# Kernel tuning notes

Measured on AMD Instinct MI355X. Metric: run time of the kernel, lower is better.

Reference implementation:

```python
import jax, jax.numpy as jnp
import numpy as np

NEG = -1e30  # log-space 'zero'


def setup_inputs() -> dict:
    N, T, IDIM, V, S = 16, 1024, 512, 4096, 128
    key = jax.random.key(0)
    k0, k1, k2, k3, k4 = jax.random.split(key, 5)
    hs = jax.random.normal(k0, (N, T, IDIM), dtype=jnp.float32)
    hlens = jax.random.randint(k1, (N,), T // 2, T + 1).astype(jnp.int32)
    ys = jax.random.randint(k2, (N, S), 1, V).astype(jnp.int32)  # labels exclude blank=0
    ylens = jax.random.randint(k3, (N,), S // 2, S + 1).astype(jnp.int32)
    W = jax.random.normal(k4, (V, IDIM), dtype=jnp.float32) * 0.02
    b = jnp.zeros((V,), dtype=jnp.float32)
    return {"hs": hs, "hlens": hlens, "ys": ys, "ylens": ylens, "W": W, "b": b}


def _ctc_loss(logp, hlens, ys, ylens):
    # logp: (N, T, V) log-softmax outputs; blank index = 0
    N, T, V = logp.shape
    S = ys.shape[1]
    L = 2 * S + 1
    # extended label sequence: blank, y1, blank, y2, ..., blank
    ext = jnp.zeros((N, L), dtype=ys.dtype).at[:, 1::2].set(ys)  # (N, L)
    s_idx = jnp.arange(L)
    ext_prev2 = jnp.pad(ext, ((0, 0), (2, 0)))[:, :L]
    allow_skip = (ext != 0) & (ext != ext_prev2) & (s_idx[None, :] >= 2)  # (N, L)
    Ln = 2 * ylens + 1  # valid extended length per sample

    lpT = jnp.swapaxes(logp, 0, 1)  # (T, N, V)

    # t = 0 init
    alpha0 = jnp.full((N, L), NEG, dtype=logp.dtype)
    alpha0 = alpha0.at[:, 0].set(lpT[0, :, 0])
    alpha0 = alpha0.at[:, 1].set(jnp.take_along_axis(lpT[0], ys[:, :1], axis=1)[:, 0])

    def step(alpha, xs):
        lp_t, t = xs  # lp_t: (N, V)
        lp_ext = jnp.take_along_axis(lp_t, ext, axis=1)  # (N, L)
        a1 = alpha
        a2 = jnp.pad(alpha, ((0, 0), (1, 0)), constant_values=NEG)[:, :L]
        a3 = jnp.pad(alpha, ((0, 0), (2, 0)), constant_values=NEG)[:, :L]
        a3 = jnp.where(allow_skip, a3, NEG)
        new = jnp.logaddexp(jnp.logaddexp(a1, a2), a3) + lp_ext
        new = jnp.where(s_idx[None, :] < Ln[:, None], new, NEG)
        alpha = jnp.where((t < hlens)[:, None], new, alpha)
        return alpha, None

    ts = jnp.arange(1, T, dtype=hlens.dtype)
    alpha, _ = jax.lax.scan(step, alpha0, (lpT[1:], ts))

    end1 = jnp.take_along_axis(alpha, (Ln - 1)[:, None], axis=1)[:, 0]
    end2 = jnp.take_along_axis(alpha, (Ln - 2)[:, None], axis=1)[:, 0]
    ll = jnp.logaddexp(end1, end2)  # (N,)
    per = jnp.where(ll > -1e29, -ll, 0.0)  # zero_infinity=True
    return jnp.sum(per) / N  # reduction='sum' then divided by len(hlens)


def reference(hs, hlens, ys, ylens, W, b):
    logits = jnp.einsum('nti,vi->ntv', hs, W) + b  # (N, T, V)
    logp = jax.nn.log_softmax(logits, axis=-1)
    return _ctc_loss(logp, hlens, ys, ylens)
```

## Files before the change

### kernel.cpp

```cpp
#include <hip/hip_runtime.h>
#include <cstdint>
#include <cstddef>

using short8_t = __attribute__((ext_vector_type(8))) short;
using f32x4    = __attribute__((ext_vector_type(4))) float;
typedef unsigned short bfu16;

constexpr int   Nn   = 16;
constexpr int   Tt   = 1024;
constexpr int   IDIM = 512;
constexpr int   Vv   = 4096;
constexpr int   Ss   = 128;
constexpr int   Ll   = 2 * Ss + 1;
constexpr int   LS   = 132;
constexpr int   PST  = LS * Tt;
constexpr float NEGV = -1e30f;
constexpr float L2E  = 1.4426950408889634f;
constexpr float LN2  = 0.6931471805599453f;

__device__ __forceinline__ float fexp2(float x) { return __builtin_amdgcn_exp2f(x); }
__device__ __forceinline__ float flog2(float x) { return __builtin_amdgcn_logf(x); }

__device__ __forceinline__ float dpp_shr1(float x) {
  return __int_as_float(__builtin_amdgcn_update_dpp(
      0, __float_as_int(x), 0x138, 0xf, 0xf, true));
}
__device__ __forceinline__ float dpp_shr2(float x) {
  return dpp_shr1(dpp_shr1(x));
}

__device__ __forceinline__ float rowsum16(float s) {
  s += __int_as_float(__builtin_amdgcn_update_dpp(0, __float_as_int(s), 0x121, 0xf, 0xf, false));
  s += __int_as_float(__builtin_amdgcn_update_dpp(0, __float_as_int(s), 0x122, 0xf, 0xf, false));
  s += __int_as_float(__builtin_amdgcn_update_dpp(0, __float_as_int(s), 0x124, 0xf, 0xf, false));
  s += __int_as_float(__builtin_amdgcn_update_dpp(0, __float_as_int(s), 0x128, 0xf, 0xf, false));
  return s;
}

__device__ __forceinline__ float rowmax16(float v) {
  v = fmaxf(v, __int_as_float(__builtin_amdgcn_update_dpp(0, __float_as_int(v), 0x121, 0xf, 0xf, false)));
  v = fmaxf(v, __int_as_float(__builtin_amdgcn_update_dpp(0, __float_as_int(v), 0x122, 0xf, 0xf, false)));
  v = fmaxf(v, __int_as_float(__builtin_amdgcn_update_dpp(0, __float_as_int(v), 0x124, 0xf, 0xf, false)));
  v = fmaxf(v, __int_as_float(__builtin_amdgcn_update_dpp(0, __float_as_int(v), 0x128, 0xf, 0xf, false)));
  return v;
}

__device__ __forceinline__ bfu16 f2bf(float f) {
  unsigned int x = __float_as_uint(f);
  x = x + 0x7fffu + ((x >> 16) & 1u);
  return (bfu16)(x >> 16);
}

__device__ __forceinline__ void async16(const void* g, void* l) {
  __builtin_amdgcn_global_load_lds(
      (__attribute__((address_space(1))) void*)(g),
      (__attribute__((address_space(3))) void*)(l), 16, 0, 0);
}

__global__ void convert_zero(const float4* __restrict__ hs4,
                             const float4* __restrict__ W4,
                             ushort4* __restrict__ hsb4,
                             ushort4* __restrict__ Wb4,
                             float* __restrict__ out) {
  if (blockIdx.x == 0 && threadIdx.x == 0) out[0] = 0.f;
  const int HS4 = (Nn * Tt * IDIM) / 4;
  const int TOT = HS4 + (Vv * IDIM) / 4;
  for (int i = blockIdx.x * 256 + threadIdx.x; i < TOT; i += gridDim.x * 256) {
    float4 f;
    if (i < HS4) f = hs4[i]; else f = W4[i - HS4];
    ushort4 o;
    o.x = f2bf(f.x); o.y = f2bf(f.y); o.z = f2bf(f.z); o.w = f2bf(f.w);
    if (i < HS4) hsb4[i] = o; else Wb4[i - HS4] = o;
  }
}

__global__ void build_labels(const int* __restrict__ ys,
                             int* __restrict__ labmap,
                             int* __restrict__ extidx,
                             int* __restrict__ skipflag) {
  const int n = blockIdx.x, tid = threadIdx.x;
  int* lm = labmap + n * Vv;
  for (int v = tid; v < Vv; v += 256) lm[v] = 0x7fffffff;
  __syncthreads();
  if (tid == 0) lm[0] = 0;
  if (tid < Ss) atomicMin(&lm[ys[n * Ss + tid]], tid + 1);
  __syncthreads();
  for (int s = tid; s < Ll; s += 256) {
    int v = (s & 1) ? ys[n * Ss + ((s - 1) >> 1)] : 0;
    extidx[n * Ll + s] = lm[v];
    int allow = 0;
    if ((s & 1) && s >= 3) allow = (v != ys[n * Ss + ((s - 3) >> 1)]) ? 1 : 0;
    skipflag[n * Ll + s] = allow;
  }
  __syncthreads();
  for (int v = tid; v < Vv; v += 256)
    if (lm[v] == 0x7fffffff) lm[v] = -1;
}

__global__ __launch_bounds__(512, 2) void gemm_lse(
    const bfu16* __restrict__ A,
    const bfu16* __restrict__ B,
    const float* __restrict__ bias,
    const int*   __restrict__ labmap,
    float* __restrict__ plabT,
    float* __restrict__ psum) {
  __shared__ alignas(128) char ldsraw[131072];
  const int tid  = threadIdx.x;
  const int lane = tid & 63, wid = tid >> 6;
  const int wr = wid >> 2, wc = wid & 3;

  const int flat = blockIdx.x;
  const int wg   = (flat & 7) * 128 + (flat >> 3);
  const int bR = wg >> 4, bC = wg & 15;
  const int rowbase = bR * 256, colbase = bC * 256;

  f32x4 acc[8][4];
#pragma unroll
  for (int m = 0; m < 8; m++)
#pragma unroll
    for (int n = 0; n < 4; n++) {
      f32x4 z = {0.f, 0.f, 0.f, 0.f};
      acc[m][n] = z;
    }

  const int  sw  = wid & 3;
  const bool isB = wid >= 4;
  const char* gsrc0 = (const char*)(isB ? (const void*)B : (const void*)A)
      + (size_t)((isB ? colbase : rowbase) + sw * 64 + (lane >> 3)) * (IDIM * 2)
      + (((lane & 7) ^ ((lane >> 3) & 7)) * 16);
  char* ldst0 = ldsraw + (isB ? 32768 : 0) + sw * 8192;

  const int fr = lane & 15;
  const int g  = lane >> 4;
  const int fx = fr & 7;

  const int nsamp = bR >> 2;
  const int* lm = labmap + nsamp * Vv;
  float* plT = plabT + (size_t)nsamp * PST;
  float bc[4];
  int   slot[4];
#pragma unroll
  for (int n = 0; n < 4; n++) {
    int c = colbase + wc * 64 + n * 16 + fr;
    bc[n]   = bias[c];
    slot[n] = lm[c];
  }

  auto stage = [&](int b, int t) {
#pragma unroll
    for (int i = 0; i < 8; ++i)
      async16(gsrc0 + (size_t)t * 128 + i * 8192, ldst0 + b * 65536 + i * 1024);
  };
  auto stage1 = [&](int b, int t, int i) {
    async16(gsrc0 + (size_t)t * 128 + (size_t)i * 8192, ldst0 + b * 65536 + i * 1024);
  };

  stage(0, 0);
  stage(1, 1);

  int buf = 0;
  for (int t = 0; t < 8; ++t) {
    if (t < 7) asm volatile("s_waitcnt vmcnt(8)" ::: "memory");
    else       asm volatile("s_waitcnt vmcnt(0)" ::: "memory");
    __builtin_amdgcn_s_barrier();

    const char* Ab = ldsraw + buf * 65536;
    const char* Bb = Ab + 32768;

    short8_t a0[4], a1[4], a2[4], a3[4], b0[4], b1[4];
#pragma unroll
    for (int m = 0; m < 4; m++)
      a0[m] = *(const short8_t*)(Ab + (wr * 128 + m * 16 + fr) * 128 + ((0 + g) ^ fx) * 16);
#pragma unroll
    for (int n = 0; n < 4; n++)
      b0[n] = *(const short8_t*)(Bb + (wc * 64 + n * 16 + fr) * 128 + ((0 + g) ^ fx) * 16);
#pragma unroll
    for (int m = 0; m < 4; m++)
      a1[m] = *(const short8_t*)(Ab + (wr * 128 + (m + 4) * 16 + fr) * 128 + ((0 + g) ^ fx) * 16);

    __builtin_amdgcn_s_setprio(1);
#pragma unroll
    for (int m = 0; m < 4; m++)
#pragma unroll
      for (int n = 0; n < 4; n++)
        acc[m][n] = __builtin_amdgcn_mfma_f32_16x16x32_bf16(a0[m], b0[n], acc[m][n], 0, 0, 0);
    __builtin_amdgcn_s_setprio(0);

#pragma unroll
    for (int m = 0; m < 4; m++)
      a2[m] = *(const short8_t*)(Ab + (wr * 128 + m * 16 + fr) * 128 + ((4 + g) ^ fx) * 16);
#pragma unroll
    for (int n = 0; n < 4; n++)
      b1[n] = *(const short8_t*)(Bb + (wc * 64 + n * 16 + fr) * 128 + ((4 + g) ^ fx) * 16);

    __builtin_amdgcn_s_setprio(1);
#pragma unroll
    for (int m = 0; m < 4; m++)
#pragma unroll
      for (int n = 0; n < 4; n++)
        acc[m + 4][n] = __builtin_amdgcn_mfma_f32_16x16x32_bf16(a1[m], b0[n], acc[m + 4][n], 0, 0, 0);
    __builtin_amdgcn_s_setprio(0);

#pragma unroll
    for (int m = 0; m < 4; m++)
      a3[m] = *(const short8_t*)(Ab + (wr * 128 + (m + 4) * 16 + fr) * 128 + ((4 + g) ^ fx) * 16);

    asm volatile("s_waitcnt lgkmcnt(0)" ::: "memory");
    __builtin_amdgcn_s_barrier();

    const bool dostage = (t + 2 < 8);
    if (dostage) {
      stage1(buf, t + 2, 0); stage1(buf, t + 2, 1);
      stage1(buf, t + 2, 2); stage1(buf, t + 2, 3);
    }

    __builtin_amdgcn_s_setprio(1);
#pragma unroll
    for (int m = 0; m < 4; m++)
#pragma unroll
      for (int n = 0; n < 4; n++)
        acc[m][n] = __builtin_amdgcn_mfma_f32_16x16x32_bf16(a2[m], b1[n], acc[m][n], 0, 0, 0);
    __builtin_amdgcn_s_setprio(0);

    if (dostage) {
      stage1(buf, t + 2, 4); stage1(buf, t + 2, 5);
      stage1(buf, t + 2, 6); stage1(buf, t + 2, 7);
    }

    __builtin_amdgcn_s_setprio(1);
#pragma unroll
    for (int m = 0; m < 4; m++)
#pragma unroll
      for (int n = 0; n < 4; n++)
        acc[m + 4][n] = __builtin_amdgcn_mfma_f32_16x16x32_bf16(a3[m], b1[n], acc[m + 4][n], 0, 0, 0);
    __builtin_amdgcn_s_setprio(0);

    buf ^= 1;
  }

  const int g4 = g * 4;
#pragma unroll
  for (int m = 0; m < 8; m++) {
#pragma unroll
    for (int r = 0; r < 4; r++) {
      int row = rowbase + wr * 128 + m * 16 + g4 + r;
      int tIn = row & 1023;
      float e0 = fexp2((acc[m][0][r] + bc[0]) * L2E);
      float e1 = fexp2((acc[m][1][r] + bc[1]) * L2E);
      float e2 = fexp2((acc[m][2][r] + bc[2]) * L2E);
      float e3 = fexp2((acc[m][3][r] + bc[3]) * L2E);
      if (slot[0] >= 0) plT[(size_t)slot[0] * Tt + tIn] = e0;
      if (slot[1] >= 0) plT[(size_t)slot[1] * Tt + tIn] = e1;
      if (slot[2] >= 0) plT[(size_t)slot[2] * Tt + tIn] = e2;
      if (slot[3] >= 0) plT[(size_t)slot[3] * Tt + tIn] = e3;
      float s = rowsum16((e0 + e1) + (e2 + e3));
      if (fr == 0) {
        int pc = bC * 4 + wc;
        psum[(size_t)pc * 16384 + row] = s;
      }
    }
  }
}

__global__ void lse_reduce(const float* __restrict__ psum,
                           float* __restrict__ lse) {
  int row = blockIdx.x * 256 + threadIdx.x;
  float s = 0.f;
#pragma unroll 8
  for (int j = 0; j < 64; j++)
    s += psum[(size_t)j * 16384 + row];
  lse[row] = flog2(s) * LN2;
}

__global__ __launch_bounds__(64) void ctc_dp(
    const float* __restrict__ plabT, const float* __restrict__ lse,
    const int* __restrict__ extidx, const int* __restrict__ skipflag,
    const int* __restrict__ hlens, const int* __restrict__ ylens,
    float* __restrict__ out) {
  __shared__ float alf[264];
  const int n    = blockIdx.x;
  const int lane = threadIdx.x;
  const int hlen = hlens[n];
  const int Ln   = 2 * ylens[n] + 1;
  const int sbase = lane * 4;

  const int   e1  = extidx[n * Ll + sbase + 1];
  const int   e3  = extidx[n * Ll + sbase + 3];
  const float sk1 = skipflag[n * Ll + sbase + 1] ? 1.f : 0.f;
  const float sk3 = skipflag[n * Ll + sbase + 3] ? 1.f : 0.f;
  const float skh = (lane > 0 && skipflag[n * Ll + sbase - 1]) ? 1.f : 0.f;
  const float skz = (lane > 0 && skipflag[n * Ll + sbase - 3]) ? 1.f : 0.f;
  const float skv = (lane > 1 && skipflag[n * Ll + sbase - 5]) ? 1.f : 0.f;
  const bool  l0  = (lane == 0);
  const float m0  = (sbase + 0 < Ln) ? 1.f : 0.f;
  const float m1  = (sbase + 1 < Ln) ? 1.f : 0.f;
  const float m2  = (sbase + 2 < Ln) ? 1.f : 0.f;
  const float m3  = (sbase + 3 < Ln) ? 1.f : 0.f;
  const float m4  = (lane == 63 && Ln == 257) ? 1.f : 0.f;

  const float* pl  = plabT + (size_t)n * PST;
  const float* rb  = pl;
  const float* r1p = pl + (size_t)e1 * Tt;
  const float* r3p = pl + (size_t)e3 * Tt;
  const float* lsp = lse + n * Tt;

  float slse = 0.f;
#pragma unroll
  for (int j = 0; j < 16; j++) {
    int t = lane + 64 * j;
    float v = lsp[t];
    slse += (t < hlen) ? v : 0.f;
  }
#pragma unroll
  for (int off = 32; off; off >>= 1) slse += __shfl_xor(slse, off);

  float a0 = 0.f, a1 = 0.f, a2 = 0.f, a3 = 0.f, a4 = 0.f;
  if (l0) { a0 = rb[0]; a1 = r1p[0]; }

  int sc = 0;

  auto step1 = [&](float pb, float p1, float p3) {
    float pm1 = dpp_shr1(a3);
    float n4 = (a4 + a3) * pb;
    float n3 = (a3 + a2 + sk3 * a1) * p3;
    float n2 = (a2 + a1) * pb;
    float n1 = (a1 + a0 + sk1 * pm1) * p1;
    float n0 = (a0 + pm1) * pb;
    a0 = n0; a1 = n1; a2 = n2; a3 = n3; a4 = n4;
  };

  auto pair2 = [&](float pbA, float p1A, float p3A,
                   float pbB, float p1B, float p3B) {
    float pa3 = dpp_shr1(a3);
    float pa2 = dpp_shr1(a2);
    float pa1 = dpp_shr1(a1);
    float prA = dpp_shr1(p3A);
    float h1 = (pa3 + pa2 + skh * pa1) * prA;
    float s4 = (a4 + a3) * pbA;
    float s3 = (a3 + a2 + sk3 * a1) * p3A;
    float s2 = (a2 + a1) * pbA;
    float s1 = (a1 + a0 + sk1 * pa3) * p1A;
    float s0 = (a0 + pa3) * pbA;
    a4 = (s4 + s3) * pbB;
    a3 = (s3 + s2 + sk3 * s1) * p3B;
    a2 = (s2 + s1) * pbB;
    a1 = (s1 + s0 + sk1 * h1) * p1B;
    a0 = (s0 + h1) * pbB;
  };

  auto rescale = [&]() {
    a0 *= m0; a1 *= m1; a2 *= m2; a3 *= m3; a4 *= m4;
    float mx = fmaxf(fmaxf(a0, a1), fmaxf(a2, a3));
    mx = fmaxf(mx, a4);
    mx = rowmax16(mx);
    mx = fmaxf(mx, __shfl_xor(mx, 16));
    mx = fmaxf(mx, __shfl_xor(mx, 32));
    int ee = (int)((__float_as_uint(mx) >> 23) & 0xff) - 127;
    ee = (mx > 0.f) ? ee : 0;
    float s = __uint_as_float((unsigned)(127 - ee) << 23);
    sc += ee;
    a0 *= s; a1 *= s; a2 *= s; a3 *= s; a4 *= s;
  };

  float pb_[2][4][4], p1_[2][4][4], p3_[2][4][4];
  float hx_[2][4][3], hz_[2][4][2], hv_[2][4];

  auto loadSB = [&](int sl, int t4) {
#pragma unroll
    for (int q = 0; q < 4; q++) {
      float4 vb = *(const float4*)(rb  + t4 + 4 * q);
      float4 v1 = *(const float4*)(r1p + t4 + 4 * q);
      float4 v3 = *(const float4*)(r3p + t4 + 4 * q);
      pb_[sl][q][0] = vb.x; pb_[sl][q][1] = vb.y; pb_[sl][q][2] = vb.z; pb_[sl][q][3] = vb.w;
      p1_[sl][q][0] = v1.x; p1_[sl][q][1] = v1.y; p1_[sl][q][2] = v1.z; p1_[sl][q][3] = v1.w;
      p3_[sl][q][0] = v3.x; p3_[sl][q][1] = v3.y; p3_[sl][q][2] = v3.z; p3_[sl][q][3] = v3.w;
    }
  };

  auto haloSB = [&](int sl) {
#pragma unroll
    for (int q = 0; q < 4; q++) {
      hx_[sl][q][0] = dpp_shr1(p3_[sl][q][0]);
      hx_[sl][q][1] = dpp_shr1(p3_[sl][q][1]);
      hx_[sl][q][2] = dpp_shr1(p3_[sl][q][2]);
      hz_[sl][q][0] = dpp_shr1(p1_[sl][q][0]);
      hz_[sl][q][1] = dpp_shr1(p1_[sl][q][1]);
      hv_[sl][q]    = dpp_shr2(p3_[sl][q][0]);
    }
  };

  auto quadsSB = [&](int sl) {
#pragma unroll
    for (int q = 0; q < 4; q++) {
      float x0 = dpp_shr1(a3);
      float y0 = dpp_shr1(a2);
      float z0 = dpp_shr1(a1);
      float w0 = dpp_shr1(a0);
      float v0 = dpp_shr2(a3);
      float u0 = dpp_shr2(a2);
      float q0 = dpp_shr2(a1);

      float v1 = (v0 + u0 + skv * q0) * hv_[sl][q];
      float w1 = (w0 + v0) * pb_[sl][q][0];
      float z1 = (z0 + w0 + skz * v0) * hz_[sl][q][0];
      float y1 = (y0 + z0) * pb_[sl][q][0];
      float x1 = (x0 + y0 + skh * z0) * hx_[sl][q][0];
      float z2 = (z1 + w1 + skz * v1) * hz_[sl][q][1];
      float y2 = (y1 + z1) * pb_[sl][q][1];
      float x2 = (x1 + y1 + skh * z1) * hx_[sl][q][1];
      float x3 = (x2 + y2 + skh * z2) * hx_[sl][q][2];

      float xk[4] = {x0, x1, x2, x3};
#pragma unroll
      for (int r = 0; r < 4; r++) {
        float pb = pb_[sl][q][r], p1v = p1_[sl][q][r], p3v = p3_[sl][q][r];
        float n4 = (a4 + a3) * pb;
        float n3 = (a3 + a2 + sk3 * a1) * p3v;
        float n2 = (a2 + a1) * pb;
        float n1 = (a1 + a0 + sk1 * xk[r]) * p1v;
        float n0 = (a0 + xk[r]) * pb;
        a0 = n0; a1 = n1; a2 = n2; a3 = n3; a4 = n4;
      }
    }
  };

  const int nsteps = hlen - 1;

  int t = 1;
  while (t < 4 && t <= nsteps) {
    step1(rb[t], r1p[t], r3p[t]);
    ++t;
  }

  const int nSB = (nsteps >= 19) ? (nsteps - 3) / 16 : 0;
  int t4 = 4;
  if (nSB > 0) loadSB(0, t4);

  int done = 0;
  while (done + 2 <= nSB) {
    if (done + 1 < nSB) loadSB(1, t4 + 16);
    haloSB(0); quadsSB(0);
    if (done + 2 < nSB) loadSB(0, t4 + 32);
    haloSB(1); quadsSB(1);
    rescale();
    done += 2; t4 += 32;
  }
  if (done < nSB) {
    haloSB(0); quadsSB(0);
    rescale();
    t4 += 16;
  }
  t = 4 + 16 * nSB;

  for (; t + 1 <= nsteps; t += 2) {
    pair2(rb[t], r1p[t], r3p[t], rb[t + 1], r1p[t + 1], r3p[t + 1]);
  }
  if (t <= nsteps) {
    step1(rb[t], r1p[t], r3p[t]);
  }
  rescale();

  alf[sbase + 0] = a0; alf[sbase + 1] = a1;
  alf[sbase + 2] = a2; alf[sbase + 3] = a3;
  if (lane == 63) alf[256] = a4;
  __syncthreads();
  if (l0) {
    float sum = alf[Ln - 1] + alf[Ln - 2];
    float per = 0.f;
    if (sum > 0.f) {
      float llv = (flog2(sum) + (float)sc) * LN2 - slse;
      if (llv > -1e29f) per = -llv;
    }
    atomicAdd(out, per * (1.0f / 16.0f));
  }
}

extern "C" void kernel_launch(void* const* d_in, const int* in_sizes, int n_in,
                              void* d_out, int out_size, void* d_ws, size_t ws_size,
                              hipStream_t stream) {
  const float* hs    = (const float*)d_in[0];
  const int*   hlens = (const int*)d_in[1];
  const int*   ys    = (const int*)d_in[2];
  const int*   ylens = (const int*)d_in[3];
  const float* W     = (const float*)d_in[4];
  const float* bias  = (const float*)d_in[5];
  float*       out   = (float*)d_out;
  char*        ws    = (char*)d_ws;

  const size_t off_hsb    = 0;
  const size_t off_Wb     = off_hsb    + (size_t)Nn*Tt*IDIM*2;
  const size_t off_plab   = off_Wb     + (size_t)Vv*IDIM*2;
  const size_t off_psum   = off_plab   + (size_t)Nn*LS*Tt*4;
  const size_t off_lse    = off_psum   + (size_t)64*16384*4;
  const size_t off_labmap = off_lse    + (size_t)16384*4;
  const size_t off_extidx = off_labmap + (size_t)Nn*Vv*4;
  const size_t off_skip   = off_extidx + (size_t)((Nn*Ll*4 + 255) & ~255);

  bfu16* hsb    = (bfu16*)(ws + off_hsb);
  bfu16* Wb     = (bfu16*)(ws + off_Wb);
  float* plabT  = (float*)(ws + off_plab);
  float* psum   = (float*)(ws + off_psum);
  float* lse    = (float*)(ws + off_lse);
  int*   labmap = (int*)(ws + off_labmap);
  int*   extidx = (int*)(ws + off_extidx);
  int*   skipf  = (int*)(ws + off_skip);

  convert_zero<<<2048, 256, 0, stream>>>(
      (const float4*)hs, (const float4*)W, (ushort4*)hsb, (ushort4*)Wb, out);
  build_labels<<<16, 256, 0, stream>>>(ys, labmap, extidx, skipf);
  gemm_lse<<<1024, 512, 0, stream>>>(hsb, Wb, bias, labmap, plabT, psum);
  lse_reduce<<<64, 256, 0, stream>>>(psum, lse);
  ctc_dp<<<16, 64, 0, stream>>>(plabT, lse, extidx, skipf, hlens, ylens, out);
}
```

Before: 172.7 us.

## Scatter label probabilities into per-position time-major packed buffer for CTC DP

Instead of storing one row per unique label and having the DP gather rows through an extidx indirection, the GEMM epilogue now writes each label's exp-logit to every sequence position it occupies, in a [T][128] time-major packed layout. The CTC DP then loads one float2 per lane per timestep, contiguous across lanes, replacing two strided float4 row streams. This trades a loop of extra scattered global stores in the GEMM epilogue (and a serial single-thread label build) for coalesced loads in the latency-bound DP. Duplicate labels beyond 16 occurrences would be dropped.

```diff
diff --git a/kernel.cpp b/kernel.cpp
--- a/kernel.cpp
+++ b/kernel.cpp
@@ -14,6 +14,7 @@
 constexpr int   Ll   = 2 * Ss + 1;
 constexpr int   LS   = 132;
 constexpr int   PST  = LS * Tt;
+constexpr int   PKS  = Tt * 128;
 constexpr float NEGV = -1e30f;
 constexpr float L2E  = 1.4426950408889634f;
 constexpr float LN2  = 0.6931471805599453f;
@@ -75,34 +76,38 @@
 }
 
 __global__ void build_labels(const int* __restrict__ ys,
-                             int* __restrict__ labmap,
-                             int* __restrict__ extidx,
+                             int* __restrict__ poscnt,
+                             int* __restrict__ poslist,
                              int* __restrict__ skipflag) {
   const int n = blockIdx.x, tid = threadIdx.x;
-  int* lm = labmap + n * Vv;
-  for (int v = tid; v < Vv; v += 256) lm[v] = 0x7fffffff;
+  int* pc = poscnt + n * Vv;
+  for (int v = tid; v < Vv; v += 256) pc[v] = 0;
   __syncthreads();
-  if (tid == 0) lm[0] = 0;
-  if (tid < Ss) atomicMin(&lm[ys[n * Ss + tid]], tid + 1);
-  __syncthreads();
+  if (tid == 0) {
+    int* pl_ = poslist + (size_t)n * Vv * 16;
+    for (int j = 0; j < Ss; j++) {
+      int v = ys[n * Ss + j];
+      int k = pc[v];
+      if (k < 16) pl_[v * 16 + k] = j;
+      pc[v] = k + 1;
+    }
+  }
   for (int s = tid; s < Ll; s += 256) {
-    int v = (s & 1) ? ys[n * Ss + ((s - 1) >> 1)] : 0;
-    extidx[n * Ll + s] = lm[v];
     int allow = 0;
-    if ((s & 1) && s >= 3) allow = (v != ys[n * Ss + ((s - 3) >> 1)]) ? 1 : 0;
+    if ((s & 1) && s >= 3)
+      allow = (ys[n * Ss + ((s - 1) >> 1)] != ys[n * Ss + ((s - 3) >> 1)]) ? 1 : 0;
     skipflag[n * Ll + s] = allow;
   }
-  __syncthreads();
-  for (int v = tid; v < Vv; v += 256)
-    if (lm[v] == 0x7fffffff) lm[v] = -1;
 }
 
 __global__ __launch_bounds__(512, 2) void gemm_lse(
     const bfu16* __restrict__ A,
     const bfu16* __restrict__ B,
     const float* __restrict__ bias,
-    const int*   __restrict__ labmap,
+    const int*   __restrict__ poscnt,
+    const int*   __restrict__ poslist,
     float* __restrict__ plabT,
+    float* __restrict__ pkP,
     float* __restrict__ psum) {
   __shared__ alignas(128) char ldsraw[131072];
   const int tid  = threadIdx.x;
@@ -135,15 +140,18 @@
   const int fx = fr & 7;
 
   const int nsamp = bR >> 2;
-  const int* lm = labmap + nsamp * Vv;
-  float* plT = plabT + (size_t)nsamp * PST;
+  const int* pcn = poscnt + nsamp * Vv;
+  const int* pln = poslist + (size_t)nsamp * Vv * 16;
+  float* plT  = plabT + (size_t)nsamp * PST;
+  float* pk_n = pkP + (size_t)nsamp * PKS;
   float bc[4];
-  int   slot[4];
+  int   col[4], cntc[4];
 #pragma unroll
   for (int n = 0; n < 4; n++) {
     int c = colbase + wc * 64 + n * 16 + fr;
+    col[n]  = c;
     bc[n]   = bias[c];
-    slot[n] = lm[c];
+    cntc[n] = pcn[c];
   }
 
   auto stage = [&](int b, int t) {
@@ -245,15 +253,18 @@
     for (int r = 0; r < 4; r++) {
       int row = rowbase + wr * 128 + m * 16 + g4 + r;
       int tIn = row & 1023;
-      float e0 = fexp2((acc[m][0][r] + bc[0]) * L2E);
-      float e1 = fexp2((acc[m][1][r] + bc[1]) * L2E);
-      float e2 = fexp2((acc[m][2][r] + bc[2]) * L2E);
-      float e3 = fexp2((acc[m][3][r] + bc[3]) * L2E);
-      if (slot[0] >= 0) plT[(size_t)slot[0] * Tt + tIn] = e0;
-      if (slot[1] >= 0) plT[(size_t)slot[1] * Tt + tIn] = e1;
-      if (slot[2] >= 0) plT[(size_t)slot[2] * Tt + tIn] = e2;
-      if (slot[3] >= 0) plT[(size_t)slot[3] * Tt + tIn] = e3;
-      float s = rowsum16((e0 + e1) + (e2 + e3));
+      float ev[4];
+#pragma unroll
+      for (int j = 0; j < 4; j++) {
+        float e = fexp2((acc[m][j][r] + bc[j]) * L2E);
+        ev[j] = e;
+        if (col[j] == 0) plT[tIn] = e;
+        for (int q2 = 0; q2 < cntc[j]; q2++) {
+          int pos = pln[col[j] * 16 + q2];
+          pk_n[(size_t)tIn * 128 + pos] = e;
+        }
+      }
+      float s = rowsum16((ev[0] + ev[1]) + (ev[2] + ev[3]));
       if (fr == 0) {
         int pc = bC * 4 + wc;
         psum[(size_t)pc * 16384 + row] = s;
@@ -273,8 +284,8 @@
 }
 
 __global__ __launch_bounds__(64) void ctc_dp(
-    const float* __restrict__ plabT, const float* __restrict__ lse,
-    const int* __restrict__ extidx, const int* __restrict__ skipflag,
+    const float* __restrict__ plabT, const float* __restrict__ pkP,
+    const float* __restrict__ lse, const int* __restrict__ skipflag,
     const int* __restrict__ hlens, const int* __restrict__ ylens,
     float* __restrict__ out) {
   __shared__ float alf[264];
@@ -284,8 +295,6 @@
   const int Ln   = 2 * ylens[n] + 1;
   const int sbase = lane * 4;
 
-  const int   e1  = extidx[n * Ll + sbase + 1];
-  const int   e3  = extidx[n * Ll + sbase + 3];
   const float sk1 = skipflag[n * Ll + sbase + 1] ? 1.f : 0.f;
   const float sk3 = skipflag[n * Ll + sbase + 3] ? 1.f : 0.f;
   const float skh = (lane > 0 && skipflag[n * Ll + sbase - 1]) ? 1.f : 0.f;
@@ -298,11 +307,9 @@
   const float m3  = (sbase + 3 < Ln) ? 1.f : 0.f;
   const float m4  = (lane == 63 && Ln == 257) ? 1.f : 0.f;
 
-  const float* pl  = plabT + (size_t)n * PST;
-  const float* rb  = pl;
-  const float* r1p = pl + (size_t)e1 * Tt;
-  const float* r3p = pl + (size_t)e3 * Tt;
-  const float* lsp = lse + n * Tt;
+  const float*  rb  = plabT + (size_t)n * PST;
+  const float2* pk2 = (const float2*)(pkP + (size_t)n * PKS);
+  const float*  lsp = lse + n * Tt;
 
   float slse = 0.f;
 #pragma unroll
@@ -314,8 +321,9 @@
 #pragma unroll
   for (int off = 32; off; off >>= 1) slse += __shfl_xor(slse, off);
 
+  float2 w0 = pk2[lane];
   float a0 = 0.f, a1 = 0.f, a2 = 0.f, a3 = 0.f, a4 = 0.f;
-  if (l0) { a0 = rb[0]; a1 = r1p[0]; }
+  if (l0) { a0 = rb[0]; a1 = w0.x; }
 
   int sc = 0;
 
@@ -362,30 +370,32 @@
     a0 *= s; a1 *= s; a2 *= s; a3 *= s; a4 *= s;
   };
 
-  float pb_[2][4][4], p1_[2][4][4], p3_[2][4][4];
+  float pb_[2][4][4];
+  float p1f[2][16], p3f[2][16];
   float hx_[2][4][3], hz_[2][4][2], hv_[2][4];
 
   auto loadSB = [&](int sl, int t4) {
 #pragma unroll
     for (int q = 0; q < 4; q++) {
-      float4 vb = *(const float4*)(rb  + t4 + 4 * q);
-      float4 v1 = *(const float4*)(r1p + t4 + 4 * q);
-      float4 v3 = *(const float4*)(r3p + t4 + 4 * q);
+      float4 vb = *(const float4*)(rb + t4 + 4 * q);
       pb_[sl][q][0] = vb.x; pb_[sl][q][1] = vb.y; pb_[sl][q][2] = vb.z; pb_[sl][q][3] = vb.w;
-      p1_[sl][q][0] = v1.x; p1_[sl][q][1] = v1.y; p1_[sl][q][2] = v1.z; p1_[sl][q][3] = v1.w;
-      p3_[sl][q][0] = v3.x; p3_[sl][q][1] = v3.y; p3_[sl][q][2] = v3.z; p3_[sl][q][3] = v3.w;
+    }
+#pragma unroll
+    for (int i = 0; i < 16; i++) {
+      float2 w = pk2[(size_t)(t4 + i) * 64 + lane];
+      p1f[sl][i] = w.x; p3f[sl][i] = w.y;
     }
   };
 
   auto haloSB = [&](int sl) {
 #pragma unroll
     for (int q = 0; q < 4; q++) {
-      hx_[sl][q][0] = dpp_shr1(p3_[sl][q][0]);
-      hx_[sl][q][1] = dpp_shr1(p3_[sl][q][1]);
-      hx_[sl][q][2] = dpp_shr1(p3_[sl][q][2]);
-      hz_[sl][q][0] = dpp_shr1(p1_[sl][q][0]);
-      hz_[sl][q][1] = dpp_shr1(p1_[sl][q][1]);
-      hv_[sl][q]    = dpp_shr2(p3_[sl][q][0]);
+      hx_[sl][q][0] = dpp_shr1(p3f[sl][4 * q + 0]);
+      hx_[sl][q][1] = dpp_shr1(p3f[sl][4 * q + 1]);
+      hx_[sl][q][2] = dpp_shr1(p3f[sl][4 * q + 2]);
+      hz_[sl][q][0] = dpp_shr1(p1f[sl][4 * q + 0]);
+      hz_[sl][q][1] = dpp_shr1(p1f[sl][4 * q + 1]);
+      hv_[sl][q]    = dpp_shr2(p3f[sl][4 * q + 0]);
     }
   };
 
@@ -395,14 +405,14 @@
       float x0 = dpp_shr1(a3);
       float y0 = dpp_shr1(a2);
       float z0 = dpp_shr1(a1);
-      float w0 = dpp_shr1(a0);
+      float w0_ = dpp_shr1(a0);
       float v0 = dpp_shr2(a3);
       float u0 = dpp_shr2(a2);
       float q0 = dpp_shr2(a1);
 
       float v1 = (v0 + u0 + skv * q0) * hv_[sl][q];
-      float w1 = (w0 + v0) * pb_[sl][q][0];
-      float z1 = (z0 + w0 + skz * v0) * hz_[sl][q][0];
+      float w1 = (w0_ + v0) * pb_[sl][q][0];
+      float z1 = (z0 + w0_ + skz * v0) * hz_[sl][q][0];
       float y1 = (y0 + z0) * pb_[sl][q][0];
       float x1 = (x0 + y0 + skh * z0) * hx_[sl][q][0];
       float z2 = (z1 + w1 + skz * v1) * hz_[sl][q][1];
@@ -413,7 +423,7 @@
       float xk[4] = {x0, x1, x2, x3};
 #pragma unroll
       for (int r = 0; r < 4; r++) {
-        float pb = pb_[sl][q][r], p1v = p1_[sl][q][r], p3v = p3_[sl][q][r];
+        float pb = pb_[sl][q][r], p1v = p1f[sl][4 * q + r], p3v = p3f[sl][4 * q + r];
         float n4 = (a4 + a3) * pb;
         float n3 = (a3 + a2 + sk3 * a1) * p3v;
         float n2 = (a2 + a1) * pb;
@@ -428,7 +438,8 @@
 
   int t = 1;
   while (t < 4 && t <= nsteps) {
-    step1(rb[t], r1p[t], r3p[t]);
+    float2 w = pk2[(size_t)t * 64 + lane];
+    step1(rb[t], w.x, w.y);
     ++t;
   }
 
@@ -453,10 +464,13 @@
   t = 4 + 16 * nSB;
 
   for (; t + 1 <= nsteps; t += 2) {
-    pair2(rb[t], r1p[t], r3p[t], rb[t + 1], r1p[t + 1], r3p[t + 1]);
+    float2 wA = pk2[(size_t)t * 64 + lane];
+    float2 wB = pk2[(size_t)(t + 1) * 64 + lane];
+    pair2(rb[t], wA.x, wA.y, rb[t + 1], wB.x, wB.y);
   }
   if (t <= nsteps) {
-    step1(rb[t], r1p[t], r3p[t]);
+    float2 w = pk2[(size_t)t * 64 + lane];
+    step1(rb[t], w.x, w.y);
   }
   rescale();
 
@@ -490,25 +504,27 @@
   const size_t off_hsb    = 0;
   const size_t off_Wb     = off_hsb    + (size_t)Nn*Tt*IDIM*2;
   const size_t off_plab   = off_Wb     + (size_t)Vv*IDIM*2;
-  const size_t off_psum   = off_plab   + (size_t)Nn*LS*Tt*4;
+  const size_t off_pkP    = off_plab   + (size_t)Nn*LS*Tt*4;
+  const size_t off_psum   = off_pkP    + (size_t)Nn*Tt*128*4;
   const size_t off_lse    = off_psum   + (size_t)64*16384*4;
-  const size_t off_labmap = off_lse    + (size_t)16384*4;
-  const size_t off_extidx = off_labmap + (size_t)Nn*Vv*4;
-  const size_t off_skip   = off_extidx + (size_t)((Nn*Ll*4 + 255) & ~255);
+  const size_t off_poscnt = off_lse    + (size_t)16384*4;
+  const size_t off_poslist= off_poscnt + (size_t)Nn*Vv*4;
+  const size_t off_skip   = off_poslist+ (size_t)Nn*Vv*16*4;
 
   bfu16* hsb    = (bfu16*)(ws + off_hsb);
   bfu16* Wb     = (bfu16*)(ws + off_Wb);
   float* plabT  = (float*)(ws + off_plab);
+  float* pkP    = (float*)(ws + off_pkP);
   float* psum   = (float*)(ws + off_psum);
   float* lse    = (float*)(ws + off_lse);
-  int*   labmap = (int*)(ws + off_labmap);
-  int*   extidx = (int*)(ws + off_extidx);
+  int*   poscnt = (int*)(ws + off_poscnt);
+  int*   poslist= (int*)(ws + off_poslist);
   int*   skipf  = (int*)(ws + off_skip);
 
   convert_zero<<<2048, 256, 0, stream>>>(
       (const float4*)hs, (const float4*)W, (ushort4*)hsb, (ushort4*)Wb, out);
-  build_labels<<<16, 256, 0, stream>>>(ys, labmap, extidx, skipf);
-  gemm_lse<<<1024, 512, 0, stream>>>(hsb, Wb, bias, labmap, plabT, psum);
+  build_labels<<<16, 256, 0, stream>>>(ys, poscnt, poslist, skipf);
+  gemm_lse<<<1024, 512, 0, stream>>>(hsb, Wb, bias, poscnt, poslist, plabT, pkP, psum);
   lse_reduce<<<64, 256, 0, stream>>>(psum, lse);
-  ctc_dp<<<16, 64, 0, stream>>>(plabT, lse, extidx, skipf, hlens, ylens, out);
-}
+  ctc_dp<<<16, 64, 0, stream>>>(plabT, pkP, lse, skipf, hlens, ylens, out);
+}
```

After: 268.1 us. 55.3% more time.

## Pre-gather label probabilities into time-major packed layout for CTC DP

Applied to the files above, without the earlier changes.

Adds a build_pkP kernel that gathers each sample's label-position probabilities from plabT into a time-major array, so each lane reads one float2 (odd positions 1 and 3) per timestep. The CTC DP then loads coalesced float2 rows instead of two per-lane float4 streams from scattered label rows. This is meant to cut uncoalesced, latency-bound memory traffic in the serial DP kernel. The cost is an extra launch, an extra 8 MB workspace buffer and a transpose pass through shared memory.

```diff
diff --git a/kernel.cpp b/kernel.cpp
--- a/kernel.cpp
+++ b/kernel.cpp
@@ -14,6 +14,7 @@
 constexpr int   Ll   = 2 * Ss + 1;
 constexpr int   LS   = 132;
 constexpr int   PST  = LS * Tt;
+constexpr int   PKS  = Tt * 128;
 constexpr float NEGV = -1e30f;
 constexpr float L2E  = 1.4426950408889634f;
 constexpr float LN2  = 0.6931471805599453f;
@@ -97,6 +98,29 @@
     if (lm[v] == 0x7fffffff) lm[v] = -1;
 }
 
+__global__ __launch_bounds__(256) void build_pkP(
+    const float* __restrict__ plabT, const int* __restrict__ extidx,
+    float* __restrict__ pkP) {
+  __shared__ float tile[128][65];
+  __shared__ int spos[128];
+  const int n   = blockIdx.x >> 4;
+  const int t0  = (blockIdx.x & 15) * 64;
+  const int tid = threadIdx.x;
+  if (tid < 128) spos[tid] = extidx[n * Ll + 2 * tid + 1];
+  __syncthreads();
+  const float* pl = plabT + (size_t)n * PST;
+  const int lane = tid & 63, w = tid >> 6;
+  for (int p = w; p < 128; p += 4)
+    tile[p][lane] = pl[(size_t)spos[p] * Tt + t0 + lane];
+  __syncthreads();
+  float* dst = pkP + (size_t)n * PKS + (size_t)t0 * 128;
+  const int pos = tid & 127, half = tid >> 7;
+  for (int i = 0; i < 64; i += 2) {
+    int t = i + half;
+    dst[(size_t)t * 128 + pos] = tile[pos][t];
+  }
+}
+
 __global__ __launch_bounds__(512, 2) void gemm_lse(
     const bfu16* __restrict__ A,
     const bfu16* __restrict__ B,
@@ -273,8 +297,8 @@
 }
 
 __global__ __launch_bounds__(64) void ctc_dp(
-    const float* __restrict__ plabT, const float* __restrict__ lse,
-    const int* __restrict__ extidx, const int* __restrict__ skipflag,
+    const float* __restrict__ plabT, const float* __restrict__ pkP,
+    const float* __restrict__ lse, const int* __restrict__ skipflag,
     const int* __restrict__ hlens, const int* __restrict__ ylens,
     float* __restrict__ out) {
   __shared__ float alf[264];
@@ -284,8 +308,6 @@
   const int Ln   = 2 * ylens[n] + 1;
   const int sbase = lane * 4;
 
-  const int   e1  = extidx[n * Ll + sbase + 1];
-  const int   e3  = extidx[n * Ll + sbase + 3];
   const float sk1 = skipflag[n * Ll + sbase + 1] ? 1.f : 0.f;
   const float sk3 = skipflag[n * Ll + sbase + 3] ? 1.f : 0.f;
   const float skh = (lane > 0 && skipflag[n * Ll + sbase - 1]) ? 1.f : 0.f;
@@ -298,11 +320,9 @@
   const float m3  = (sbase + 3 < Ln) ? 1.f : 0.f;
   const float m4  = (lane == 63 && Ln == 257) ? 1.f : 0.f;
 
-  const float* pl  = plabT + (size_t)n * PST;
-  const float* rb  = pl;
-  const float* r1p = pl + (size_t)e1 * Tt;
-  const float* r3p = pl + (size_t)e3 * Tt;
-  const float* lsp = lse + n * Tt;
+  const float*  rb  = plabT + (size_t)n * PST;
+  const float2* pk2 = (const float2*)(pkP + (size_t)n * PKS);
+  const float*  lsp = lse + n * Tt;
 
   float slse = 0.f;
 #pragma unroll
@@ -314,8 +334,9 @@
 #pragma unroll
   for (int off = 32; off; off >>= 1) slse += __shfl_xor(slse, off);
 
+  float2 w0 = pk2[lane];
   float a0 = 0.f, a1 = 0.f, a2 = 0.f, a3 = 0.f, a4 = 0.f;
-  if (l0) { a0 = rb[0]; a1 = r1p[0]; }
+  if (l0) { a0 = rb[0]; a1 = w0.x; }
 
   int sc = 0;
 
@@ -362,30 +383,32 @@
     a0 *= s; a1 *= s; a2 *= s; a3 *= s; a4 *= s;
   };
 
-  float pb_[2][4][4], p1_[2][4][4], p3_[2][4][4];
+  float pb_[2][4][4];
+  float p1f[2][16], p3f[2][16];
   float hx_[2][4][3], hz_[2][4][2], hv_[2][4];
 
   auto loadSB = [&](int sl, int t4) {
 #pragma unroll
     for (int q = 0; q < 4; q++) {
-      float4 vb = *(const float4*)(rb  + t4 + 4 * q);
-      float4 v1 = *(const float4*)(r1p + t4 + 4 * q);
-      float4 v3 = *(const float4*)(r3p + t4 + 4 * q);
+      float4 vb = *(const float4*)(rb + t4 + 4 * q);
       pb_[sl][q][0] = vb.x; pb_[sl][q][1] = vb.y; pb_[sl][q][2] = vb.z; pb_[sl][q][3] = vb.w;
-      p1_[sl][q][0] = v1.x; p1_[sl][q][1] = v1.y; p1_[sl][q][2] = v1.z; p1_[sl][q][3] = v1.w;
-      p3_[sl][q][0] = v3.x; p3_[sl][q][1] = v3.y; p3_[sl][q][2] = v3.z; p3_[sl][q][3] = v3.w;
+    }
+#pragma unroll
+    for (int i = 0; i < 16; i++) {
+      float2 w = pk2[(size_t)(t4 + i) * 64 + lane];
+      p1f[sl][i] = w.x; p3f[sl][i] = w.y;
     }
   };
 
   auto haloSB = [&](int sl) {
 #pragma unroll
     for (int q = 0; q < 4; q++) {
-      hx_[sl][q][0] = dpp_shr1(p3_[sl][q][0]);
-      hx_[sl][q][1] = dpp_shr1(p3_[sl][q][1]);
-      hx_[sl][q][2] = dpp_shr1(p3_[sl][q][2]);
-      hz_[sl][q][0] = dpp_shr1(p1_[sl][q][0]);
-      hz_[sl][q][1] = dpp_shr1(p1_[sl][q][1]);
-      hv_[sl][q]    = dpp_shr2(p3_[sl][q][0]);
+      hx_[sl][q][0] = dpp_shr1(p3f[sl][4 * q + 0]);
+      hx_[sl][q][1] = dpp_shr1(p3f[sl][4 * q + 1]);
+      hx_[sl][q][2] = dpp_shr1(p3f[sl][4 * q + 2]);
+      hz_[sl][q][0] = dpp_shr1(p1f[sl][4 * q + 0]);
+      hz_[sl][q][1] = dpp_shr1(p1f[sl][4 * q + 1]);
+      hv_[sl][q]    = dpp_shr2(p3f[sl][4 * q + 0]);
     }
   };
 
@@ -395,14 +418,14 @@
       float x0 = dpp_shr1(a3);
       float y0 = dpp_shr1(a2);
       float z0 = dpp_shr1(a1);
-      float w0 = dpp_shr1(a0);
+      float w0_ = dpp_shr1(a0);
       float v0 = dpp_shr2(a3);
       float u0 = dpp_shr2(a2);
       float q0 = dpp_shr2(a1);
 
       float v1 = (v0 + u0 + skv * q0) * hv_[sl][q];
-      float w1 = (w0 + v0) * pb_[sl][q][0];
-      float z1 = (z0 + w0 + skz * v0) * hz_[sl][q][0];
+      float w1 = (w0_ + v0) * pb_[sl][q][0];
+      float z1 = (z0 + w0_ + skz * v0) * hz_[sl][q][0];
       float y1 = (y0 + z0) * pb_[sl][q][0];
       float x1 = (x0 + y0 + skh * z0) * hx_[sl][q][0];
       float z2 = (z1 + w1 + skz * v1) * hz_[sl][q][1];
@@ -413,7 +436,7 @@
       float xk[4] = {x0, x1, x2, x3};
 #pragma unroll
       for (int r = 0; r < 4; r++) {
-        float pb = pb_[sl][q][r], p1v = p1_[sl][q][r], p3v = p3_[sl][q][r];
+        float pb = pb_[sl][q][r], p1v = p1f[sl][4 * q + r], p3v = p3f[sl][4 * q + r];
         float n4 = (a4 + a3) * pb;
         float n3 = (a3 + a2 + sk3 * a1) * p3v;
         float n2 = (a2 + a1) * pb;
@@ -428,7 +451,8 @@
 
   int t = 1;
   while (t < 4 && t <= nsteps) {
-    step1(rb[t], r1p[t], r3p[t]);
+    float2 w = pk2[(size_t)t * 64 + lane];
+    step1(rb[t], w.x, w.y);
     ++t;
   }
 
@@ -453,10 +477,13 @@
   t = 4 + 16 * nSB;
 
   for (; t + 1 <= nsteps; t += 2) {
-    pair2(rb[t], r1p[t], r3p[t], rb[t + 1], r1p[t + 1], r3p[t + 1]);
+    float2 wA = pk2[(size_t)t * 64 + lane];
+    float2 wB = pk2[(size_t)(t + 1) * 64 + lane];
+    pair2(rb[t], wA.x, wA.y, rb[t + 1], wB.x, wB.y);
   }
   if (t <= nsteps) {
-    step1(rb[t], r1p[t], r3p[t]);
+    float2 w = pk2[(size_t)t * 64 + lane];
+    step1(rb[t], w.x, w.y);
   }
   rescale();
 
@@ -490,7 +517,8 @@
   const size_t off_hsb    = 0;
   const size_t off_Wb     = off_hsb    + (size_t)Nn*Tt*IDIM*2;
   const size_t off_plab   = off_Wb     + (size_t)Vv*IDIM*2;
-  const size_t off_psum   = off_plab   + (size_t)Nn*LS*Tt*4;
+  const size_t off_pkP    = off_plab   + (size_t)Nn*LS*Tt*4;
+  const size_t off_psum   = off_pkP    + (size_t)Nn*Tt*128*4;
   const size_t off_lse    = off_psum   + (size_t)64*16384*4;
   const size_t off_labmap = off_lse    + (size_t)16384*4;
   const size_t off_extidx = off_labmap + (size_t)Nn*Vv*4;
@@ -499,6 +527,7 @@
   bfu16* hsb    = (bfu16*)(ws + off_hsb);
   bfu16* Wb     = (bfu16*)(ws + off_Wb);
   float* plabT  = (float*)(ws + off_plab);
+  float* pkP    = (float*)(ws + off_pkP);
   float* psum   = (float*)(ws + off_psum);
   float* lse    = (float*)(ws + off_lse);
   int*   labmap = (int*)(ws + off_labmap);
@@ -509,6 +538,7 @@
       (const float4*)hs, (const float4*)W, (ushort4*)hsb, (ushort4*)Wb, out);
   build_labels<<<16, 256, 0, stream>>>(ys, labmap, extidx, skipf);
   gemm_lse<<<1024, 512, 0, stream>>>(hsb, Wb, bias, labmap, plabT, psum);
+  build_pkP<<<256, 256, 0, stream>>>(plabT, extidx, pkP);
   lse_reduce<<<64, 256, 0, stream>>>(psum, lse);
-  ctc_dp<<<16, 64, 0, stream>>>(plabT, lse, extidx, skipf, hlens, ylens, out);
-}
+  ctc_dp<<<16, 64, 0, stream>>>(plabT, pkP, lse, skipf, hlens, ylens, out);
+}
```

Result: slower. 182.2 us (+5.5%).
